# Kernel optimization log

Measured on AMD Instinct MI355X. Metric: run time of the kernel, lower is better.

Reference implementation:

```python
import jax, jax.numpy as jnp
import numpy as np

B, M_IN, M_OUT, C = 4, 16, 32, 32


def setup_inputs() -> dict:
    key = jax.random.key(0)
    kx, = jax.random.split(key, 1)
    x = jax.random.normal(kx, (B, M_IN, C, C, C, C), dtype=jnp.float32)
    init = jnp.ones((M_IN, M_OUT), dtype=jnp.float32) / M_IN
    return {"x": x, "alpha": init, "beta": init, "gamma": init, "delta": init}


def reference(x, alpha, beta, gamma, delta):
    # Faithful to the torch code's permute+sum bookkeeping (note: torch's
    # permute(0,1,3,2,4,5).sum((2,4,5)) reduces ORIGINAL axes (3,4,5),
    # keeping original axis 2 -- identical to s1).
    s1 = x.sum(axis=(3, 4, 5))  # (B, M_in, C), keeps axis 2
    s2 = x.sum(axis=(3, 4, 5))  # same as s1 (permuted-sum in torch keeps axis 2)
    s3 = x.sum(axis=(2, 4, 5))  # keeps axis 3
    s4 = x.sum(axis=(2, 3, 5))  # keeps axis 4
    s = jnp.stack([s1, s2, s3, s4], axis=2)            # (B, M_in, 4, C)
    w = jnp.stack([alpha, beta, gamma, delta], axis=2)  # (M_in, M_out, 4)
    # 'bmic,mnd->bnic': sums over m and w's stack axis d; keeps s's stack axis i.
    out = jnp.einsum('bmic,mnd->bnic', s, w)            # (B, M_out, 4, C)
    return out
```

## Files before the change

kernel.cpp:

```cpp
#include <hip/hip_runtime.h>


#define P3_OFF 2048
#define P4_OFF (2048 + 65536)

__global__ __launch_bounds__(256) void reduce_k(const float* __restrict__ x,
                                                float* __restrict__ ws) {
    const int t   = threadIdx.x;
    const int bid = blockIdx.x;
    const int lane = t & 63;
    const int wv   = t >> 6;

    __shared__ float lds3[4][32];
    __shared__ float lds4[32];
    __shared__ float lds1[4];

    const float4* xv = (const float4*)x + (size_t)bid * 8192;

    float total = 0.0f;
    #pragma unroll
    for (int it = 0; it < 32; ++it) {
        float4 v = xv[it * 256 + t];
        float s = (v.x + v.y) + (v.z + v.w);
        total += s;
        #pragma unroll
        for (int off = 1; off < 64; off <<= 1)
            s += __shfl_xor(s, off, 64);
        if (lane == 0) lds3[wv][it] = s;
    }

    float g = total;
    g += __shfl_xor(g, 1, 64);
    g += __shfl_xor(g, 2, 64);
    g += __shfl_xor(g, 4, 64);
    if ((t & 7) == 0) lds4[t >> 3] = g;

    float wsum = g;
    wsum += __shfl_xor(wsum, 8, 64);
    wsum += __shfl_xor(wsum, 16, 64);
    wsum += __shfl_xor(wsum, 32, 64);
    if (lane == 0) lds1[wv] = wsum;

    __syncthreads();

    if (t < 32) {
        float v3 = lds3[0][t] + lds3[1][t] + lds3[2][t] + lds3[3][t];
        ws[P3_OFF + bid * 32 + t] = v3;
        ws[P4_OFF + bid * 32 + t] = lds4[t];
    }
    if (t == 0)
        ws[bid] = lds1[0] + lds1[1] + lds1[2] + lds1[3];
}

__global__ __launch_bounds__(256) void finalize_k(const float* __restrict__ ws,
                                                  const float* __restrict__ alpha,
                                                  const float* __restrict__ beta,
                                                  const float* __restrict__ gamma,
                                                  const float* __restrict__ delta,
                                                  float* __restrict__ out) {
    __shared__ float W[512];
    __shared__ float S[16][32];
    const int t  = threadIdx.x;
    const int b  = blockIdx.x >> 2;
    const int i4 = blockIdx.x & 3;

    #pragma unroll
    for (int i = t; i < 512; i += 256)
        W[i] = alpha[i] + beta[i] + gamma[i] + delta[i];

    if (i4 <= 1) {
        #pragma unroll
        for (int i = t; i < 512; i += 256) {
            int m = i >> 5, c = i & 31;
            S[m][c] = ws[(b * 16 + m) * 32 + c];
        }
    } else {
        const float* p = ws + (i4 == 2 ? P3_OFF : P4_OFF);
        #pragma unroll
        for (int i = t; i < 512; i += 256) {
            int m = i >> 5, c = i & 31;
            const float* q = p + (b * 16 + m) * 1024 + c;
            float acc = 0.0f;
            #pragma unroll
            for (int c2 = 0; c2 < 32; ++c2)
                acc += q[c2 * 32];
            S[m][c] = acc;
        }
    }
    __syncthreads();

    #pragma unroll
    for (int k = 0; k < 4; ++k) {
        int idx = k * 256 + t;
        int n = idx >> 5, c = idx & 31;
        float acc = 0.0f;
        #pragma unroll
        for (int m = 0; m < 16; ++m)
            acc += S[m][c] * W[m * 32 + n];
        out[((b * 32 + n) * 4 + i4) * 32 + c] = acc;
    }
}

extern "C" void kernel_launch(void* const* d_in, const int* in_sizes, int n_in,
                              void* d_out, int out_size, void* d_ws, size_t ws_size,
                              hipStream_t stream) {
    const float* x     = (const float*)d_in[0];
    const float* alpha = (const float*)d_in[1];
    const float* beta  = (const float*)d_in[2];
    const float* gamma = (const float*)d_in[3];
    const float* delta = (const float*)d_in[4];
    float* out = (float*)d_out;
    float* ws  = (float*)d_ws;

    reduce_k<<<2048, 256, 0, stream>>>(x, ws);
    finalize_k<<<16, 256, 0, stream>>>(ws, alpha, beta, gamma, delta, out);
}
```

Measured before the change: 365.6 us.

## Restructure reduce so each wave owns contiguous rows, cutting shuffle reductions

Each wave now processes a contiguous quarter of the block's slab, loading four float4 per lane per iteration. That cuts the per-row 64-lane butterfly reductions from 32 to 8 per wave. Per-row sums are written straight to the workspace instead of going through LDS, and the s1 total is no longer stored but recomputed in finalize by summing 32 partials. This lowers the shuffle and instruction count in the memory-bound reduce, at the cost of uncoalesced scalar stores from lane 0 and extra work in the small finalize kernel.

```diff
diff --git a/kernel.cpp b/kernel.cpp
--- a/kernel.cpp
+++ b/kernel.cpp
@@ -1,55 +1,61 @@
 #include <hip/hip_runtime.h>
 
 
-#define P3_OFF 2048
-#define P4_OFF (2048 + 65536)
+#define P3_OFF 0
+#define P4_OFF 65536
 
 __global__ __launch_bounds__(256) void reduce_k(const float* __restrict__ x,
                                                 float* __restrict__ ws) {
-    const int t   = threadIdx.x;
-    const int bid = blockIdx.x;
+    const int t    = threadIdx.x;
+    const int bid  = blockIdx.x;
     const int lane = t & 63;
     const int wv   = t >> 6;
 
-    __shared__ float lds3[4][32];
-    __shared__ float lds4[32];
-    __shared__ float lds1[4];
+    __shared__ float lds4[4][32];
 
-    const float4* xv = (const float4*)x + (size_t)bid * 8192;
+    const float4* xv = (const float4*)x + (size_t)bid * 8192 + wv * 2048;
 
-    float total = 0.0f;
-    #pragma unroll
-    for (int it = 0; it < 32; ++it) {
-        float4 v = xv[it * 256 + t];
-        float s = (v.x + v.y) + (v.z + v.w);
-        total += s;
+    float acc0 = 0.f, acc1 = 0.f, acc2 = 0.f, acc3 = 0.f;
+
+    #pragma unroll 2
+    for (int it = 0; it < 8; ++it) {
+        const float4* row = xv + it * 256;
+        float4 f0 = row[lane];
+        float4 f1 = row[lane + 64];
+        float4 f2 = row[lane + 128];
+        float4 f3 = row[lane + 192];
+        float v0 = (f0.x + f0.y) + (f0.z + f0.w);
+        float v1 = (f1.x + f1.y) + (f1.z + f1.w);
+        float v2 = (f2.x + f2.y) + (f2.z + f2.w);
+        float v3 = (f3.x + f3.y) + (f3.z + f3.w);
+        acc0 += v0; acc1 += v1; acc2 += v2; acc3 += v3;
+        float s = (v0 + v1) + (v2 + v3);
         #pragma unroll
         for (int off = 1; off < 64; off <<= 1)
             s += __shfl_xor(s, off, 64);
-        if (lane == 0) lds3[wv][it] = s;
+        if (lane == 0)
+            ws[P3_OFF + bid * 32 + wv * 8 + it] = s;
     }
 
-    float g = total;
-    g += __shfl_xor(g, 1, 64);
-    g += __shfl_xor(g, 2, 64);
-    g += __shfl_xor(g, 4, 64);
-    if ((t & 7) == 0) lds4[t >> 3] = g;
-
-    float wsum = g;
-    wsum += __shfl_xor(wsum, 8, 64);
-    wsum += __shfl_xor(wsum, 16, 64);
-    wsum += __shfl_xor(wsum, 32, 64);
-    if (lane == 0) lds1[wv] = wsum;
-
+    #pragma unroll
+    for (int off = 1; off < 8; off <<= 1) {
+        acc0 += __shfl_xor(acc0, off, 64);
+        acc1 += __shfl_xor(acc1, off, 64);
+        acc2 += __shfl_xor(acc2, off, 64);
+        acc3 += __shfl_xor(acc3, off, 64);
+    }
+    if ((lane & 7) == 0) {
+        int g = lane >> 3;
+        lds4[wv][g]      = acc0;
+        lds4[wv][g + 8]  = acc1;
+        lds4[wv][g + 16] = acc2;
+        lds4[wv][g + 24] = acc3;
+    }
     __syncthreads();
 
-    if (t < 32) {
-        float v3 = lds3[0][t] + lds3[1][t] + lds3[2][t] + lds3[3][t];
-        ws[P3_OFF + bid * 32 + t] = v3;
-        ws[P4_OFF + bid * 32 + t] = lds4[t];
-    }
-    if (t == 0)
-        ws[bid] = lds1[0] + lds1[1] + lds1[2] + lds1[3];
+    if (t < 32)
+        ws[P4_OFF + bid * 32 + t] =
+            lds4[0][t] + lds4[1][t] + lds4[2][t] + lds4[3][t];
 }
 
 __global__ __launch_bounds__(256) void finalize_k(const float* __restrict__ ws,
@@ -72,7 +78,12 @@
         #pragma unroll
         for (int i = t; i < 512; i += 256) {
             int m = i >> 5, c = i & 31;
-            S[m][c] = ws[(b * 16 + m) * 32 + c];
+            const float* q = ws + P3_OFF + (b * 16 + m) * 1024 + c * 32;
+            float acc = 0.0f;
+            #pragma unroll
+            for (int k = 0; k < 32; ++k)
+                acc += q[k];
+            S[m][c] = acc;
         }
     } else {
         const float* p = ws + (i4 == 2 ? P3_OFF : P4_OFF);
```

New measurement: 366.6 us. About the same (+0.3%).
